# Kernel optimization log

Hardware: AMD Instinct MI355X
Metric: run time of the kernel (lower is better)

## Reference

```python
import jax, jax.numpy as jnp
import numpy as np

N = 50000   # total nodes across batch of graphs
E = 600000  # edges (avg degree 12)
D = 128     # feature dim
L = 3       # GNN layers
B = 64      # number of graphs


def setup_inputs() -> dict:
    key = jax.random.key(0)
    ks = jax.random.split(key, 9)
    x = jax.random.normal(ks[0], (N, D), dtype=jnp.float32)
    edge_index = jax.random.randint(ks[1], (2, E), 0, N)
    batch = jnp.sort(jax.random.randint(ks[2], (N,), 0, B))
    # hard one-hot architecture gates (output of ST gumbel-softmax)
    z_agg = jax.nn.one_hot(jax.random.randint(ks[3], (L,), 0, 3), 3, dtype=jnp.float32)
    z_pool = jax.nn.one_hot(jax.random.randint(ks[4], (), 0, 3), 3, dtype=jnp.float32)
    scale = 1.0 / np.sqrt(D)
    W1 = jax.random.normal(ks[5], (L, D, D), dtype=jnp.float32) * scale
    b1 = jnp.zeros((L, D), dtype=jnp.float32)
    W2 = jax.random.normal(ks[6], (L, D, D), dtype=jnp.float32) * scale
    b2 = jnp.zeros((L, D), dtype=jnp.float32)
    return {"x": x, "edge_index": edge_index, "batch": batch,
            "z_agg": z_agg, "z_pool": z_pool,
            "W1": W1, "b1": b1, "W2": W2, "b2": b2}


def reference(x, edge_index, batch, z_agg, z_pool, W1, b1, W2, b2):
    src, dst = edge_index[0], edge_index[1]
    ones_e = jnp.ones((E,), dtype=x.dtype)
    deg = jax.ops.segment_sum(ones_e, dst, num_segments=N)          # [N]
    deg_c = jnp.maximum(deg, 1.0)[:, None]
    has_nb = (deg > 0)[:, None]

    for l in range(L):
        msg = x[src]                                                # [E, D] gather
        s = jax.ops.segment_sum(msg, dst, num_segments=N)           # sum aggr
        m = s / deg_c                                               # mean aggr
        mx = jax.ops.segment_max(msg, dst, num_segments=N)          # max aggr
        mx = jnp.where(has_nb, mx, 0.0)                             # PyG fills empty with 0
        agg = z_agg[l, 0] * s + z_agg[l, 1] * m + z_agg[l, 2] * mx
        # combine='sum' then FeedForwardNetwork: Linear->relu->Linear
        h = x + agg
        h = jnp.maximum(h @ W1[l] + b1[l], 0.0)
        h = h @ W2[l] + b2[l]
        # act='relu', layer_connect='skip_sum'
        x = x + jnp.maximum(h, 0.0)

    # global pooling mixture over batch vector
    ps = jax.ops.segment_sum(x, batch, num_segments=B)              # [B, D]
    cnt = jax.ops.segment_sum(jnp.ones((N,), x.dtype), batch, num_segments=B)
    pm = ps / jnp.maximum(cnt, 1.0)[:, None]
    pmx = jax.ops.segment_max(x, batch, num_segments=B)
    pmx = jnp.where((cnt > 0)[:, None], pmx, 0.0)
    return z_pool[0] * ps + z_pool[1] * pm + z_pool[2] * pmx
```

## Files before the change

kernel.cpp:

```cpp
#include <hip/hip_runtime.h>
#include <cfloat>

#define DD 128
#define NLAYERS 3
#define NPB 128
#define SCHUNK 1024

typedef short bf16x8 __attribute__((ext_vector_type(8)));
typedef float f32x4 __attribute__((ext_vector_type(4)));

__device__ __forceinline__ unsigned short f2b(float f) {
    unsigned u = __float_as_uint(f);
    u += 0x7fffu + ((u >> 16) & 1u);
    return (unsigned short)(u >> 16);
}
__device__ __forceinline__ float b2f(unsigned short b) {
    return __uint_as_float(((unsigned)b) << 16);
}

__device__ __forceinline__ unsigned enc_f(float f) {
    unsigned b = __float_as_uint(f);
    return (b & 0x80000000u) ? ~b : (b | 0x80000000u);
}
__device__ __forceinline__ float dec_f(unsigned u) {
    return __uint_as_float((u & 0x80000000u) ? (u & 0x7fffffffu) : ~u);
}

__global__ void convert_init_kernel(const float* __restrict__ x_in,
                                    unsigned short* __restrict__ xb,
                                    const float* __restrict__ W1s, const float* __restrict__ W2s,
                                    unsigned short* __restrict__ Wb1s,
                                    unsigned short* __restrict__ Wb2s,
                                    int* __restrict__ deg,
                                    float* __restrict__ ps, unsigned* __restrict__ pmx,
                                    int* __restrict__ cnt,
                                    int n4, int nN, int nBD, int nB, int per, int xbBlocks) {
    if ((int)blockIdx.x < xbBlocks) {
        int i = blockIdx.x * 256 + threadIdx.x;
        if (i < n4) {
            float4 v = ((const float4*)x_in)[i];
            ushort4 b;
            b.x = f2b(v.x); b.y = f2b(v.y); b.z = f2b(v.z); b.w = f2b(v.w);
            ((ushort4*)xb)[i] = b;
        }
        if (i < nN) deg[i] = 0;
        if (i < nBD) { ps[i] = 0.f; pmx[i] = 0u; }
        if (i < nB) cnt[i] = 0;
    } else {
        int idx = (blockIdx.x - xbBlocks) * 256 + threadIdx.x;
        if (idx >= 2 * per) return;
        const float* W = (idx < per) ? W1s : W2s;
        unsigned short* Wb = (idx < per) ? Wb1s : Wb2s;
        if (idx >= per) idx -= per;
        int lane = idx & 63;
        int rest = idx >> 6;
        int ks = rest & 3; rest >>= 2;
        int nt = rest & 7;
        int l  = rest >> 3;
        int n = nt * 16 + (lane & 15);
        int kbase = ks * 32 + (lane >> 4) * 8;
        const float* Wl = W + (size_t)l * DD * DD;
        unsigned short* dst = Wb + (size_t)l * DD * DD + ((size_t)(nt * 4 + ks) * 64 + lane) * 8;
#pragma unroll
        for (int j = 0; j < 8; ++j) dst[j] = f2b(Wl[(size_t)(kbase + j) * DD + n]);
    }
}


__global__ void deg_kernel(const int* __restrict__ dst, int* __restrict__ deg, int nE) {
    int e = blockIdx.x * blockDim.x + threadIdx.x;
    if (e < nE) atomicAdd(&deg[dst[e]], 1);
}

__global__ __launch_bounds__(256) void scan_sum_kernel(const int* __restrict__ deg,
                                                       int* __restrict__ bsum, int nN) {
    int t = threadIdx.x;
    int base = blockIdx.x * SCHUNK + t * 4;
    int v = 0;
#pragma unroll
    for (int k = 0; k < 4; ++k) { int i = base + k; if (i < nN) v += deg[i]; }
    for (int off = 32; off; off >>= 1) v += __shfl_down(v, off, 64);
    __shared__ int wsum[4];
    if ((t & 63) == 0) wsum[t >> 6] = v;
    __syncthreads();
    if (t == 0) bsum[blockIdx.x] = wsum[0] + wsum[1] + wsum[2] + wsum[3];
}

__global__ __launch_bounds__(256) void scan_apply_kernel(const int* __restrict__ deg,
                                                         const int* __restrict__ bsum,
                                                         int* __restrict__ row_ptr,
                                                         int nN, int G) {
    __shared__ int sh[256];
    __shared__ int sh2[256];
    int t = threadIdx.x;
    int base = blockIdx.x * SCHUNK + t * 4;
    int d0 = 0, d1 = 0, d2 = 0, d3 = 0;
    if (base + 0 < nN) d0 = deg[base + 0];
    if (base + 1 < nN) d1 = deg[base + 1];
    if (base + 2 < nN) d2 = deg[base + 2];
    if (base + 3 < nN) d3 = deg[base + 3];
    int tsum = d0 + d1 + d2 + d3;
    sh[t] = tsum;
    sh2[t] = (t < G) ? bsum[t] : 0;
    __syncthreads();
    for (int off = 1; off < 256; off <<= 1) {
        int o  = (t >= off) ? sh[t - off]  : 0;
        int o2 = (t >= off) ? sh2[t - off] : 0;
        __syncthreads();
        sh[t] += o; sh2[t] += o2;
        __syncthreads();
    }
    int bb = (blockIdx.x > 0) ? sh2[blockIdx.x - 1] : 0;
    int run = bb + sh[t] - tsum;
    if (base + 0 < nN) row_ptr[base + 0] = run;           run += d0;
    if (base + 1 < nN) row_ptr[base + 1] = run;           run += d1;
    if (base + 2 < nN) row_ptr[base + 2] = run;           run += d2;
    if (base + 3 < nN) row_ptr[base + 3] = run;
    if (blockIdx.x == G - 1 && t == 0) row_ptr[nN] = sh2[G - 1];
}

__global__ void fill_kernel(const int* __restrict__ src, const int* __restrict__ dst,
                            const int* __restrict__ row_ptr, int* __restrict__ deg,
                            int* __restrict__ csr_src, int nE) {
    int e = blockIdx.x * blockDim.x + threadIdx.x;
    if (e >= nE) return;
    int d = dst[e];
    int pos = row_ptr[d] + atomicSub(&deg[d], 1) - 1;
    csr_src[pos] = src[e];
}

__global__ __launch_bounds__(256) void agg_combine_kernel(const unsigned short* __restrict__ xb,
                                                          const int* __restrict__ csr_src,
                                                          const int* __restrict__ row_ptr,
                                                          const float* __restrict__ z_agg_l,
                                                          unsigned short* __restrict__ h0b,
                                                          int nN) {
    int t = threadIdx.x;
    int n = blockIdx.x * 8 + (t >> 5);
    if (n >= nN) return;
    int q = t & 31;
    int start = row_ptr[n], end = row_ptr[n + 1];
    float za0 = z_agg_l[0], za1 = z_agg_l[1], za2 = z_agg_l[2];

    const ushort4* tab = (const ushort4*)xb;
    float4 sum = make_float4(0.f, 0.f, 0.f, 0.f);
    float4 mx  = make_float4(-FLT_MAX, -FLT_MAX, -FLT_MAX, -FLT_MAX);
    int last = end - 1;
    for (int e = start; e < end; e += 8) {
        int s0 = csr_src[e];
        int s1 = csr_src[e + 1 <= last ? e + 1 : last];
        int s2 = csr_src[e + 2 <= last ? e + 2 : last];
        int s3 = csr_src[e + 3 <= last ? e + 3 : last];
        int s4 = csr_src[e + 4 <= last ? e + 4 : last];
        int s5 = csr_src[e + 5 <= last ? e + 5 : last];
        int s6 = csr_src[e + 6 <= last ? e + 6 : last];
        int s7 = csr_src[e + 7 <= last ? e + 7 : last];
        ushort4 v0 = tab[(size_t)s0 * 32 + q];
        ushort4 v1 = tab[(size_t)s1 * 32 + q];
        ushort4 v2 = tab[(size_t)s2 * 32 + q];
        ushort4 v3 = tab[(size_t)s3 * 32 + q];
        ushort4 v4 = tab[(size_t)s4 * 32 + q];
        ushort4 v5 = tab[(size_t)s5 * 32 + q];
        ushort4 v6 = tab[(size_t)s6 * 32 + q];
        ushort4 v7 = tab[(size_t)s7 * 32 + q];
#define ACCP(vb, ok) { float ax=b2f(vb.x),ay=b2f(vb.y),az=b2f(vb.z),aw=b2f(vb.w); \
                  mx.x=fmaxf(mx.x,ax);mx.y=fmaxf(mx.y,ay); \
                  mx.z=fmaxf(mx.z,az);mx.w=fmaxf(mx.w,aw); \
                  if (ok) { sum.x+=ax;sum.y+=ay;sum.z+=az;sum.w+=aw; } }
        ACCP(v0, true)
        ACCP(v1, e + 1 < end)
        ACCP(v2, e + 2 < end)
        ACCP(v3, e + 3 < end)
        ACCP(v4, e + 4 < end)
        ACCP(v5, e + 5 < end)
        ACCP(v6, e + 6 < end)
        ACCP(v7, e + 7 < end)
#undef ACCP
    }
    int degn = end - start;
    float inv = 1.0f / fmaxf((float)degn, 1.0f);
    float c01 = za0 + za1 * inv;
    bool nb = (degn > 0);
    ushort4 sb = tab[(size_t)n * 32 + q];
    ushort4 r;
    r.x = f2b(b2f(sb.x) + c01 * sum.x + za2 * (nb ? mx.x : 0.f));
    r.y = f2b(b2f(sb.y) + c01 * sum.y + za2 * (nb ? mx.y : 0.f));
    r.z = f2b(b2f(sb.z) + c01 * sum.z + za2 * (nb ? mx.z : 0.f));
    r.w = f2b(b2f(sb.w) + c01 * sum.w + za2 * (nb ? mx.w : 0.f));
    ((ushort4*)(h0b + (size_t)n * DD))[q] = r;
}

__global__ __launch_bounds__(256) void fused_ffn_kernel(
        const unsigned short* __restrict__ h0b,
        const unsigned short* __restrict__ Wb1, const float* __restrict__ b1,
        const unsigned short* __restrict__ Wb2, const float* __restrict__ b2,
        const unsigned short* __restrict__ xb_in,
        unsigned short* __restrict__ xb_out, int M) {
    __shared__ char lds[64 * DD * 4];

    int t = threadIdx.x;
    int lane = t & 63;
    int w = t >> 6;
    int row0 = blockIdx.x * 64;
    int ar = row0 + w * 16 + (lane & 15);
    if (ar > M - 1) ar = M - 1;
    int g = lane >> 4;
    int colw = lane & 15;
    int rbl = w * 16 + g * 4;

    const unsigned short* Ap = h0b + (size_t)ar * DD + g * 8;
    bf16x8 a0 = *(const bf16x8*)(Ap);
    bf16x8 a1 = *(const bf16x8*)(Ap + 32);
    bf16x8 a2 = *(const bf16x8*)(Ap + 64);
    bf16x8 a3 = *(const bf16x8*)(Ap + 96);

    const bf16x8* Wv1 = (const bf16x8*)Wb1;
#pragma unroll
    for (int nt = 0; nt < 8; ++nt) {
        f32x4 acc = {0.f, 0.f, 0.f, 0.f};
        acc = __builtin_amdgcn_mfma_f32_16x16x32_bf16(a0, Wv1[(nt * 4 + 0) * 64 + lane], acc, 0, 0, 0);
        acc = __builtin_amdgcn_mfma_f32_16x16x32_bf16(a1, Wv1[(nt * 4 + 1) * 64 + lane], acc, 0, 0, 0);
        acc = __builtin_amdgcn_mfma_f32_16x16x32_bf16(a2, Wv1[(nt * 4 + 2) * 64 + lane], acc, 0, 0, 0);
        acc = __builtin_amdgcn_mfma_f32_16x16x32_bf16(a3, Wv1[(nt * 4 + 3) * 64 + lane], acc, 0, 0, 0);
        float bv = b1[nt * 16 + colw];
        int cb = (nt * 16 + colw) * 2;
#pragma unroll
        for (int i = 0; i < 4; ++i) {
            int r1 = rbl + i;
            *(unsigned short*)(lds + r1 * 256 + (cb ^ ((unsigned)(r1 & 7) << 4))) =
                f2b(fmaxf(acc[i] + bv, 0.f));
        }
    }

    int rAl = w * 16 + (lane & 15);
    unsigned swA = (unsigned)(rAl & 7) << 4;
    const char* hA = lds + rAl * 256;
    bf16x8 c0 = *(const bf16x8*)(hA + ((g * 16 +   0) ^ swA));
    bf16x8 c1 = *(const bf16x8*)(hA + ((g * 16 +  64) ^ swA));
    bf16x8 c2 = *(const bf16x8*)(hA + ((g * 16 + 128) ^ swA));
    bf16x8 c3 = *(const bf16x8*)(hA + ((g * 16 + 192) ^ swA));
    __syncthreads();

    const bf16x8* Wv2 = (const bf16x8*)Wb2;
#pragma unroll
    for (int nt = 0; nt < 8; ++nt) {
        f32x4 acc = {0.f, 0.f, 0.f, 0.f};
        acc = __builtin_amdgcn_mfma_f32_16x16x32_bf16(c0, Wv2[(nt * 4 + 0) * 64 + lane], acc, 0, 0, 0);
        acc = __builtin_amdgcn_mfma_f32_16x16x32_bf16(c1, Wv2[(nt * 4 + 1) * 64 + lane], acc, 0, 0, 0);
        acc = __builtin_amdgcn_mfma_f32_16x16x32_bf16(c2, Wv2[(nt * 4 + 2) * 64 + lane], acc, 0, 0, 0);
        acc = __builtin_amdgcn_mfma_f32_16x16x32_bf16(c3, Wv2[(nt * 4 + 3) * 64 + lane], acc, 0, 0, 0);
        float bv = b2[nt * 16 + colw];
        int cb = (nt * 16 + colw) * 4;
#pragma unroll
        for (int i = 0; i < 4; ++i) {
            int r1 = rbl + i;
            *(float*)(lds + r1 * 512 + (cb ^ ((unsigned)(r1 & 7) << 4))) =
                fmaxf(acc[i] + bv, 0.f);
        }
    }
    __syncthreads();

    int q = t & 31;
    int grp = t >> 5;
    for (int pass = 0; pass < 8; ++pass) {
        int rr = pass * 8 + grp;
        int n = row0 + rr;
        if (n < M) {
            ushort4 xv = ((const ushort4*)(xb_in + (size_t)n * DD))[q];
            float4 vv = *(const float4*)(lds + rr * 512 + ((q * 16) ^ ((unsigned)(rr & 7) << 4)));
            ushort4 b;
            b.x = f2b(b2f(xv.x) + vv.x);
            b.y = f2b(b2f(xv.y) + vv.y);
            b.z = f2b(b2f(xv.z) + vv.z);
            b.w = f2b(b2f(xv.w) + vv.w);
            ((ushort4*)(xb_out + (size_t)n * DD))[q] = b;
        }
    }
}

__global__ __launch_bounds__(256) void pool_partial_kernel(const unsigned short* __restrict__ xb,
                                                           const int* __restrict__ batch,
                                                           float* __restrict__ ps,
                                                           unsigned* __restrict__ pmx,
                                                           int* __restrict__ cnt, int nN) {
    int t = threadIdx.x;
    int q = t & 31;
    int p = t >> 5;
    int node0 = blockIdx.x * NPB;
    int nodeEnd = node0 + NPB; if (nodeEnd > nN) nodeEnd = nN;

    const ushort4* xv = (const ushort4*)xb;
    float4 sum = make_float4(0.f, 0.f, 0.f, 0.f);
    float4 mx  = make_float4(-FLT_MAX, -FLT_MAX, -FLT_MAX, -FLT_MAX);
    int count = 0, g_cur = -1;

    for (int row = node0 + p; row < nodeEnd; row += 8) {
        int g = batch[row];
        if (g != g_cur) {
            if (g_cur >= 0) {
                atomicAdd(&ps[(size_t)g_cur * DD + q * 4 + 0], sum.x);
                atomicAdd(&ps[(size_t)g_cur * DD + q * 4 + 1], sum.y);
                atomicAdd(&ps[(size_t)g_cur * DD + q * 4 + 2], sum.z);
                atomicAdd(&ps[(size_t)g_cur * DD + q * 4 + 3], sum.w);
                atomicMax(&pmx[(size_t)g_cur * DD + q * 4 + 0], enc_f(mx.x));
                atomicMax(&pmx[(size_t)g_cur * DD + q * 4 + 1], enc_f(mx.y));
                atomicMax(&pmx[(size_t)g_cur * DD + q * 4 + 2], enc_f(mx.z));
                atomicMax(&pmx[(size_t)g_cur * DD + q * 4 + 3], enc_f(mx.w));
                if (q == 0) atomicAdd(&cnt[g_cur], count);
            }
            sum = make_float4(0.f, 0.f, 0.f, 0.f);
            mx  = make_float4(-FLT_MAX, -FLT_MAX, -FLT_MAX, -FLT_MAX);
            count = 0; g_cur = g;
        }
        ushort4 vb = xv[(size_t)row * 32 + q];
        float vx = b2f(vb.x), vy = b2f(vb.y), vz = b2f(vb.z), vw = b2f(vb.w);
        sum.x += vx; sum.y += vy; sum.z += vz; sum.w += vw;
        mx.x = fmaxf(mx.x, vx); mx.y = fmaxf(mx.y, vy);
        mx.z = fmaxf(mx.z, vz); mx.w = fmaxf(mx.w, vw);
        count++;
    }
    if (g_cur >= 0) {
        atomicAdd(&ps[(size_t)g_cur * DD + q * 4 + 0], sum.x);
        atomicAdd(&ps[(size_t)g_cur * DD + q * 4 + 1], sum.y);
        atomicAdd(&ps[(size_t)g_cur * DD + q * 4 + 2], sum.z);
        atomicAdd(&ps[(size_t)g_cur * DD + q * 4 + 3], sum.w);
        atomicMax(&pmx[(size_t)g_cur * DD + q * 4 + 0], enc_f(mx.x));
        atomicMax(&pmx[(size_t)g_cur * DD + q * 4 + 1], enc_f(mx.y));
        atomicMax(&pmx[(size_t)g_cur * DD + q * 4 + 2], enc_f(mx.z));
        atomicMax(&pmx[(size_t)g_cur * DD + q * 4 + 3], enc_f(mx.w));
        if (q == 0) atomicAdd(&cnt[g_cur], count);
    }
}

__global__ void pool_final_kernel(const float* __restrict__ ps,
                                  const unsigned* __restrict__ pmx,
                                  const int* __restrict__ cnt,
                                  const float* __restrict__ z_pool,
                                  float* __restrict__ out, int total) {
    int i = blockIdx.x * blockDim.x + threadIdx.x;
    if (i >= total) return;
    int g = i >> 7;
    float zp0 = z_pool[0], zp1 = z_pool[1], zp2 = z_pool[2];
    int c = cnt[g];
    float s = ps[i];
    float pm = s / fmaxf((float)c, 1.0f);
    float pv = (c > 0) ? dec_f(pmx[i]) : 0.0f;
    out[i] = zp0 * s + zp1 * pm + zp2 * pv;
}

extern "C" void kernel_launch(void* const* d_in, const int* in_sizes, int n_in,
                              void* d_out, int out_size, void* d_ws, size_t ws_size,
                              hipStream_t stream) {
    const float* x_in   = (const float*)d_in[0];
    const int*   eidx   = (const int*)d_in[1];
    const int*   batch  = (const int*)d_in[2];
    const float* z_agg  = (const float*)d_in[3];
    const float* z_pool = (const float*)d_in[4];
    const float* W1     = (const float*)d_in[5];
    const float* b1     = (const float*)d_in[6];
    const float* W2     = (const float*)d_in[7];
    const float* b2     = (const float*)d_in[8];

    int nN = in_sizes[0] / DD;
    int nE = in_sizes[1] / 2;
    int nB = out_size / DD;
    const int* src = eidx;
    const int* dst = eidx + nE;

    char* p = (char*)d_ws;
    size_t nd = (size_t)nN * DD * sizeof(float);
    unsigned short* xb0 = (unsigned short*)p;  p += nd / 2;
    unsigned short* xbA = (unsigned short*)p;  p += nd / 2;
    unsigned short* h0b = (unsigned short*)p;  p += nd / 2;
    unsigned short* Wb1 = (unsigned short*)p;  p += (size_t)NLAYERS * DD * DD * 2;
    unsigned short* Wb2 = (unsigned short*)p;  p += (size_t)NLAYERS * DD * DD * 2;
    int* row_ptr = (int*)p;  p += (size_t)(nN + 1) * 4;
    int* deg     = (int*)p;  p += (size_t)nN * 4;
    int* csr_src = (int*)p;  p += (size_t)nE * 4 + 64;
    float*    ps  = (float*)p;    p += (size_t)nB * DD * 4;
    unsigned* pmx = (unsigned*)p; p += (size_t)nB * DD * 4;
    int*      cnt = (int*)p;      p += (size_t)nB * 4;
    int*      bsum = (int*)p;

    int G = (nN + SCHUNK - 1) / SCHUNK;

    int n4 = nN * DD / 4;
    int per = NLAYERS * 8 * 4 * 64;
    int xbBlocks = (n4 + 255) / 256;
    int wBlocks = (2 * per + 255) / 256;
    convert_init_kernel<<<xbBlocks + wBlocks, 256, 0, stream>>>(
        x_in, xb0, W1, W2, Wb1, Wb2, deg, ps, pmx, cnt,
        n4, nN, nB * DD, nB, per, xbBlocks);

    deg_kernel<<<(nE + 255) / 256, 256, 0, stream>>>(dst, deg, nE);
    scan_sum_kernel<<<G, 256, 0, stream>>>(deg, bsum, nN);
    scan_apply_kernel<<<G, 256, 0, stream>>>(deg, bsum, row_ptr, nN, G);
    fill_kernel<<<(nE + 255) / 256, 256, 0, stream>>>(src, dst, row_ptr, deg, csr_src, nE);

    int agrid = (nN + 7) / 8;
    int fgrid = (nN + 63) / 64;
    agg_combine_kernel<<<agrid, 256, 0, stream>>>(xb0, csr_src, row_ptr, z_agg + 0, h0b, nN);
    fused_ffn_kernel<<<fgrid, 256, 0, stream>>>(h0b, Wb1 + 0 * DD * DD, b1 + 0 * DD,
                                                Wb2 + 0 * DD * DD, b2 + 0 * DD,
                                                xb0, xbA, nN);
    agg_combine_kernel<<<agrid, 256, 0, stream>>>(xbA, csr_src, row_ptr, z_agg + 3, h0b, nN);
    fused_ffn_kernel<<<fgrid, 256, 0, stream>>>(h0b, Wb1 + 1 * DD * DD, b1 + 1 * DD,
                                                Wb2 + 1 * DD * DD, b2 + 1 * DD,
                                                xbA, xb0, nN);
    agg_combine_kernel<<<agrid, 256, 0, stream>>>(xb0, csr_src, row_ptr, z_agg + 6, h0b, nN);
    fused_ffn_kernel<<<fgrid, 256, 0, stream>>>(h0b, Wb1 + 2 * DD * DD, b1 + 2 * DD,
                                                Wb2 + 2 * DD * DD, b2 + 2 * DD,
                                                xb0, xbA, nN);

    pool_partial_kernel<<<(nN + NPB - 1) / NPB, 256, 0, stream>>>(xbA, batch, ps, pmx, cnt, nN);
    pool_final_kernel<<<(nB * DD + 255) / 256, 256, 0, stream>>>(ps, pmx, cnt, z_pool,
                                                                 (float*)d_out, nB * DD);
}
```

Before: 235.0 us.

## Split node features into four column panels to shrink gather working set

Stores the bf16 node feature table as four feature-column panels of 32 columns each, instead of 128-wide rows. The aggregation kernel now assigns each block a panel and 16 nodes, with 16 lanes per node reading 4 bytes each. Consecutive blocks cover different panels of the same nodes, so each panel's working set for the random neighbour gathers is smaller and should stay in L2/MALL. The FFN and pooling kernels are updated to read and write the paneled layout. The trade-off is that each gathered request is only 64 bytes and the CSR indices are re-read once per panel.

```diff
diff --git a/kernel.cpp b/kernel.cpp
--- a/kernel.cpp
+++ b/kernel.cpp
@@ -8,6 +8,7 @@
 
 typedef short bf16x8 __attribute__((ext_vector_type(8)));
 typedef float f32x4 __attribute__((ext_vector_type(4)));
+
 
 __device__ __forceinline__ unsigned short f2b(float f) {
     unsigned u = __float_as_uint(f);
@@ -41,7 +42,9 @@
             float4 v = ((const float4*)x_in)[i];
             ushort4 b;
             b.x = f2b(v.x); b.y = f2b(v.y); b.z = f2b(v.z); b.w = f2b(v.w);
-            ((ushort4*)xb)[i] = b;
+            int n = i >> 5, k = i & 31;
+            size_t PSu = (size_t)nN * 32;
+            *(ushort4*)(xb + (size_t)(k >> 3) * PSu + (size_t)n * 32 + (k & 7) * 4) = b;
         }
         if (i < nN) deg[i] = 0;
         if (i < nBD) { ps[i] = 0.f; pmx[i] = 0u; }
@@ -136,15 +139,17 @@
                                                           unsigned short* __restrict__ h0b,
                                                           int nN) {
     int t = threadIdx.x;
-    int n = blockIdx.x * 8 + (t >> 5);
+    unsigned bid = blockIdx.x;
+    int s = (bid & 7) >> 1;
+    int n = (bid >> 3) * 32 + (bid & 1) * 16 + (t >> 4);
     if (n >= nN) return;
-    int q = t & 31;
+    int l = t & 15;
+    size_t PSu = (size_t)nN * 32;
+    const unsigned short* panel = xb + (size_t)s * PSu;
     int start = row_ptr[n], end = row_ptr[n + 1];
     float za0 = z_agg_l[0], za1 = z_agg_l[1], za2 = z_agg_l[2];
 
-    const ushort4* tab = (const ushort4*)xb;
-    float4 sum = make_float4(0.f, 0.f, 0.f, 0.f);
-    float4 mx  = make_float4(-FLT_MAX, -FLT_MAX, -FLT_MAX, -FLT_MAX);
+    float sum0 = 0.f, sum1 = 0.f, mx0 = -FLT_MAX, mx1 = -FLT_MAX;
     int last = end - 1;
     for (int e = start; e < end; e += 8) {
         int s0 = csr_src[e];
@@ -155,18 +160,18 @@
         int s5 = csr_src[e + 5 <= last ? e + 5 : last];
         int s6 = csr_src[e + 6 <= last ? e + 6 : last];
         int s7 = csr_src[e + 7 <= last ? e + 7 : last];
-        ushort4 v0 = tab[(size_t)s0 * 32 + q];
-        ushort4 v1 = tab[(size_t)s1 * 32 + q];
-        ushort4 v2 = tab[(size_t)s2 * 32 + q];
-        ushort4 v3 = tab[(size_t)s3 * 32 + q];
-        ushort4 v4 = tab[(size_t)s4 * 32 + q];
-        ushort4 v5 = tab[(size_t)s5 * 32 + q];
-        ushort4 v6 = tab[(size_t)s6 * 32 + q];
-        ushort4 v7 = tab[(size_t)s7 * 32 + q];
-#define ACCP(vb, ok) { float ax=b2f(vb.x),ay=b2f(vb.y),az=b2f(vb.z),aw=b2f(vb.w); \
-                  mx.x=fmaxf(mx.x,ax);mx.y=fmaxf(mx.y,ay); \
-                  mx.z=fmaxf(mx.z,az);mx.w=fmaxf(mx.w,aw); \
-                  if (ok) { sum.x+=ax;sum.y+=ay;sum.z+=az;sum.w+=aw; } }
+        unsigned v0 = *(const unsigned*)(panel + (size_t)s0 * 32 + l * 2);
+        unsigned v1 = *(const unsigned*)(panel + (size_t)s1 * 32 + l * 2);
+        unsigned v2 = *(const unsigned*)(panel + (size_t)s2 * 32 + l * 2);
+        unsigned v3 = *(const unsigned*)(panel + (size_t)s3 * 32 + l * 2);
+        unsigned v4 = *(const unsigned*)(panel + (size_t)s4 * 32 + l * 2);
+        unsigned v5 = *(const unsigned*)(panel + (size_t)s5 * 32 + l * 2);
+        unsigned v6 = *(const unsigned*)(panel + (size_t)s6 * 32 + l * 2);
+        unsigned v7 = *(const unsigned*)(panel + (size_t)s7 * 32 + l * 2);
+#define ACCP(v, ok) { float lo = b2f((unsigned short)((v) & 0xffffu)); \
+                      float hi = b2f((unsigned short)((v) >> 16)); \
+                      mx0 = fmaxf(mx0, lo); mx1 = fmaxf(mx1, hi); \
+                      if (ok) { sum0 += lo; sum1 += hi; } }
         ACCP(v0, true)
         ACCP(v1, e + 1 < end)
         ACCP(v2, e + 2 < end)
@@ -181,13 +186,11 @@
     float inv = 1.0f / fmaxf((float)degn, 1.0f);
     float c01 = za0 + za1 * inv;
     bool nb = (degn > 0);
-    ushort4 sb = tab[(size_t)n * 32 + q];
-    ushort4 r;
-    r.x = f2b(b2f(sb.x) + c01 * sum.x + za2 * (nb ? mx.x : 0.f));
-    r.y = f2b(b2f(sb.y) + c01 * sum.y + za2 * (nb ? mx.y : 0.f));
-    r.z = f2b(b2f(sb.z) + c01 * sum.z + za2 * (nb ? mx.z : 0.f));
-    r.w = f2b(b2f(sb.w) + c01 * sum.w + za2 * (nb ? mx.w : 0.f));
-    ((ushort4*)(h0b + (size_t)n * DD))[q] = r;
+    unsigned sv = *(const unsigned*)(panel + (size_t)n * 32 + l * 2);
+    float r0 = b2f((unsigned short)(sv & 0xffffu)) + c01 * sum0 + za2 * (nb ? mx0 : 0.f);
+    float r1 = b2f((unsigned short)(sv >> 16))     + c01 * sum1 + za2 * (nb ? mx1 : 0.f);
+    unsigned outv = (unsigned)f2b(r0) | ((unsigned)f2b(r1) << 16);
+    *(unsigned*)(h0b + (size_t)s * PSu + (size_t)n * 32 + l * 2) = outv;
 }
 
 __global__ __launch_bounds__(256) void fused_ffn_kernel(
@@ -207,12 +210,12 @@
     int g = lane >> 4;
     int colw = lane & 15;
     int rbl = w * 16 + g * 4;
-
-    const unsigned short* Ap = h0b + (size_t)ar * DD + g * 8;
-    bf16x8 a0 = *(const bf16x8*)(Ap);
-    bf16x8 a1 = *(const bf16x8*)(Ap + 32);
-    bf16x8 a2 = *(const bf16x8*)(Ap + 64);
-    bf16x8 a3 = *(const bf16x8*)(Ap + 96);
+    size_t PSu = (size_t)M * 32;
+
+    bf16x8 a0 = *(const bf16x8*)(h0b + 0 * PSu + (size_t)ar * 32 + g * 8);
+    bf16x8 a1 = *(const bf16x8*)(h0b + 1 * PSu + (size_t)ar * 32 + g * 8);
+    bf16x8 a2 = *(const bf16x8*)(h0b + 2 * PSu + (size_t)ar * 32 + g * 8);
+    bf16x8 a3 = *(const bf16x8*)(h0b + 3 * PSu + (size_t)ar * 32 + g * 8);
 
     const bf16x8* Wv1 = (const bf16x8*)Wb1;
 #pragma unroll
@@ -262,18 +265,19 @@
 
     int q = t & 31;
     int grp = t >> 5;
+    size_t soff = (size_t)(q >> 3) * PSu + (q & 7) * 4;
     for (int pass = 0; pass < 8; ++pass) {
         int rr = pass * 8 + grp;
         int n = row0 + rr;
         if (n < M) {
-            ushort4 xv = ((const ushort4*)(xb_in + (size_t)n * DD))[q];
+            ushort4 xv = *(const ushort4*)(xb_in + soff + (size_t)n * 32);
             float4 vv = *(const float4*)(lds + rr * 512 + ((q * 16) ^ ((unsigned)(rr & 7) << 4)));
             ushort4 b;
             b.x = f2b(b2f(xv.x) + vv.x);
             b.y = f2b(b2f(xv.y) + vv.y);
             b.z = f2b(b2f(xv.z) + vv.z);
             b.w = f2b(b2f(xv.w) + vv.w);
-            ((ushort4*)(xb_out + (size_t)n * DD))[q] = b;
+            *(ushort4*)(xb_out + soff + (size_t)n * 32) = b;
         }
     }
 }
@@ -289,7 +293,8 @@
     int node0 = blockIdx.x * NPB;
     int nodeEnd = node0 + NPB; if (nodeEnd > nN) nodeEnd = nN;
 
-    const ushort4* xv = (const ushort4*)xb;
+    size_t PSu = (size_t)nN * 32;
+    size_t soff = (size_t)(q >> 3) * PSu + (q & 7) * 4;
     float4 sum = make_float4(0.f, 0.f, 0.f, 0.f);
     float4 mx  = make_float4(-FLT_MAX, -FLT_MAX, -FLT_MAX, -FLT_MAX);
     int count = 0, g_cur = -1;
@@ -312,7 +317,7 @@
             mx  = make_float4(-FLT_MAX, -FLT_MAX, -FLT_MAX, -FLT_MAX);
             count = 0; g_cur = g;
         }
-        ushort4 vb = xv[(size_t)row * 32 + q];
+        ushort4 vb = *(const ushort4*)(xb + soff + (size_t)row * 32);
         float vx = b2f(vb.x), vy = b2f(vb.y), vz = b2f(vb.z), vw = b2f(vb.w);
         sum.x += vx; sum.y += vy; sum.z += vz; sum.w += vw;
         mx.x = fmaxf(mx.x, vx); mx.y = fmaxf(mx.y, vy);
@@ -397,7 +402,7 @@
     scan_apply_kernel<<<G, 256, 0, stream>>>(deg, bsum, row_ptr, nN, G);
     fill_kernel<<<(nE + 255) / 256, 256, 0, stream>>>(src, dst, row_ptr, deg, csr_src, nE);
 
-    int agrid = (nN + 7) / 8;
+    int agrid = ((nN + 31) / 32) * 8;
     int fgrid = (nN + 63) / 64;
     agg_combine_kernel<<<agrid, 256, 0, stream>>>(xb0, csr_src, row_ptr, z_agg + 0, h0b, nN);
     fused_ffn_kernel<<<fgrid, 256, 0, stream>>>(h0b, Wb1 + 0 * DD * DD, b1 + 0 * DD,
```

Result: slower. 248.2 us (+5.6%).
